# Optimization experiments

Hardware: AMD Instinct MI355X
Metric: run time of the kernel (lower is better)

## Reference

```python
import jax, jax.numpy as jnp
import numpy as np

VOCAB = 50257
MASK_ID = 50256
CLIP = 20.0
GAMMA = 1.0
P_UNIFORM = float(max(np.exp(-CLIP), 0.0))
LOG_B = float(np.clip(-np.log1p((1.0 - P_UNIFORM) / P_UNIFORM * VOCAB / 2.0), -CLIP, None))
B_EXP = float(np.exp(LOG_B))
EPS = 1e-4
B_SZ, SEQ = 4, 512


def setup_inputs() -> dict:
    key = jax.random.key(0)
    k1, k2, k3 = jax.random.split(key, 3)
    input_ids = jax.random.randint(k1, (B_SZ, SEQ), 0, VOCAB)
    t = jax.random.uniform(k2, (B_SZ,), dtype=jnp.float32)
    noise = jax.random.uniform(k3, (B_SZ, SEQ, VOCAB), dtype=jnp.float32)
    return {"input_ids": input_ids, "t": t, "noise": noise}


def _coeffs(t):
    # t: [B] -> per-example blend coefficients, each [B, 1]
    t = t[:, None]
    tg = t ** GAMMA
    t1g = (1.0 - t) ** GAMMA
    c = jnp.sqrt(tg) * jnp.sqrt(t1g) * B_EXP
    C = jnp.clip(tg + t1g + (VOCAB - 2) * c, EPS, None)
    return (t1g - c) / C, c / C, tg / C  # alpha_t, c_t/C_t, t_gamma/C_t


def reference(t, noise, input_ids):
    # Fused form of probs_at_t(one_hot(input_ids), t): since prs is one-hot,
    # probs[b,s,v] = alpha*1{v==id} + c/C, then mask column overwritten to tg/C.
    alpha, cC, mC = _coeffs(t)  # [B,1] each
    col = jnp.arange(VOCAB)[None, None, :]            # [1,1,V]
    hit = col == input_ids[..., None]                 # [B,S,V]
    probs = jnp.where(col == MASK_ID, mC[..., None],
                      jnp.where(hit, (alpha + cC)[..., None], cC[..., None]))
    # Gumbel-max categorical sampling (standard sample_categorical)
    gumbel_norm = 1e-10 - jnp.log(noise + 1e-10)      # [B,S,V]
    z_t = jnp.argmax(probs / gumbel_norm, axis=-1)    # [B,S] int
    return z_t
```

## Files before the change

### kernel.cpp

```cpp
#include <hip/hip_runtime.h>
#include <stdint.h>
#include <stddef.h>


static constexpr int VOCAB   = 50257;
static constexpr int MASK_ID = 50256;
static constexpr double B_EXP_D = 2.061153622438558e-09;

__global__ __launch_bounds__(256) void hd_argmax_kernel(
    const int*   __restrict__ ids,
    const float* __restrict__ tv,
    const float* __restrict__ noise,
    int*         __restrict__ out)
{
    const int row = blockIdx.x;
    const int tid = threadIdx.x;
    const int b   = row >> 9;

    const float t   = tv[b];
    const float tg  = t;
    const float t1g = 1.0f - t;
    const float c   = sqrtf(tg) * sqrtf(t1g) * (float)B_EXP_D;
    float Cd = tg + t1g + 50255.0f * c;
    Cd = fmaxf(Cd, 1e-4f);
    const float pc = c / Cd;
    const float ph = (t1g - c) / Cd + c / Cd;
    const float pm = tg / Cd;
    const int   x  = ids[row];

    const float* __restrict__ rowp = noise + (size_t)row * (size_t)VOCAB;

    const int k     = (4 - (row & 3)) & 3;
    const int nvec  = (VOCAB - k) >> 2;
    const int tail0 = k + (nvec << 2);

    float best = -1.0f;
    int   bidx = 0;

    auto consider = [&](float u, int idx) {
        const float g = 1e-10f - logf(u + 1e-10f);
        const float p = (idx == MASK_ID) ? pm : ((idx == x) ? ph : pc);
        const float r = p / g;
        if (r > best) { best = r; bidx = idx; }
    };

    if (tid < k) consider(rowp[tid], tid);

    const float4* __restrict__ vp = reinterpret_cast<const float4*>(rowp + k);
    for (int i = tid; i < nvec; i += 256) {
        const float4 v = vp[i];
        const int base = k + (i << 2);
        consider(v.x, base);
        consider(v.y, base + 1);
        consider(v.z, base + 2);
        consider(v.w, base + 3);
    }

    if (tid < VOCAB - tail0) consider(rowp[tail0 + tid], tail0 + tid);

    #pragma unroll
    for (int off = 32; off > 0; off >>= 1) {
        const float ov = __shfl_down(best, off, 64);
        const int   oi = __shfl_down(bidx, off, 64);
        if (ov > best || (ov == best && oi < bidx)) { best = ov; bidx = oi; }
    }

    __shared__ float sv[4];
    __shared__ int   si[4];
    const int wid = tid >> 6;
    if ((tid & 63) == 0) { sv[wid] = best; si[wid] = bidx; }
    __syncthreads();
    if (tid == 0) {
        #pragma unroll
        for (int w = 1; w < 4; ++w) {
            if (sv[w] > best || (sv[w] == best && si[w] < bidx)) { best = sv[w]; bidx = si[w]; }
        }
        out[row] = bidx;
    }
}

extern "C" void kernel_launch(void* const* d_in, const int* in_sizes, int n_in,
                              void* d_out, int out_size, void* d_ws, size_t ws_size,
                              hipStream_t stream) {
    const int*   ids   = (const int*)  d_in[0];
    const float* t     = (const float*)d_in[1];
    const float* noise = (const float*)d_in[2];
    int* out = (int*)d_out;

    hd_argmax_kernel<<<dim3(2048), dim3(256), 0, stream>>>(ids, t, noise, out);
}
```

Baseline: 553.9 us.

## Replace per-element log/divide with raw noise argmax over uniform-prob columns

Because every column except the hit id and the mask column has the same probability, and p/g is monotonic in u, the scan now takes a plain argmax of the raw noise while skipping the hit id and the mask column. The log and divide are then applied only to three candidates (best uniform, hit, mask) on thread 0. This removes the transcendental and division work per element, leaving the loop bound by memory bandwidth. Tie-breaking can differ from the reference when float rounding makes distinct u values map to equal ratios.

```diff
diff --git a/kernel.cpp b/kernel.cpp
--- a/kernel.cpp
+++ b/kernel.cpp
@@ -5,6 +5,7 @@
 
 static constexpr int VOCAB   = 50257;
 static constexpr int MASK_ID = 50256;
+static constexpr int NSCAN   = VOCAB - 1;
 static constexpr double B_EXP_D = 2.061153622438558e-09;
 
 __global__ __launch_bounds__(256) void hd_argmax_kernel(
@@ -15,33 +16,19 @@
 {
     const int row = blockIdx.x;
     const int tid = threadIdx.x;
-    const int b   = row >> 9;
-
-    const float t   = tv[b];
-    const float tg  = t;
-    const float t1g = 1.0f - t;
-    const float c   = sqrtf(tg) * sqrtf(t1g) * (float)B_EXP_D;
-    float Cd = tg + t1g + 50255.0f * c;
-    Cd = fmaxf(Cd, 1e-4f);
-    const float pc = c / Cd;
-    const float ph = (t1g - c) / Cd + c / Cd;
-    const float pm = tg / Cd;
-    const int   x  = ids[row];
+    const int x   = ids[row];
 
     const float* __restrict__ rowp = noise + (size_t)row * (size_t)VOCAB;
 
-    const int k     = (4 - (row & 3)) & 3;
-    const int nvec  = (VOCAB - k) >> 2;
+    const int k    = (4 - (row & 3)) & 3;
+    const int nvec = (NSCAN - k) >> 2;
     const int tail0 = k + (nvec << 2);
 
-    float best = -1.0f;
+    float bu   = -1.0f;
     int   bidx = 0;
 
     auto consider = [&](float u, int idx) {
-        const float g = 1e-10f - logf(u + 1e-10f);
-        const float p = (idx == MASK_ID) ? pm : ((idx == x) ? ph : pc);
-        const float r = p / g;
-        if (r > best) { best = r; bidx = idx; }
+        if (u > bu && idx != x) { bu = u; bidx = idx; }
     };
 
     if (tid < k) consider(rowp[tid], tid);
@@ -56,26 +43,51 @@
         consider(v.w, base + 3);
     }
 
-    if (tid < VOCAB - tail0) consider(rowp[tail0 + tid], tail0 + tid);
+    if (tid < NSCAN - tail0) consider(rowp[tail0 + tid], tail0 + tid);
 
     #pragma unroll
     for (int off = 32; off > 0; off >>= 1) {
-        const float ov = __shfl_down(best, off, 64);
+        const float ov = __shfl_down(bu, off, 64);
         const int   oi = __shfl_down(bidx, off, 64);
-        if (ov > best || (ov == best && oi < bidx)) { best = ov; bidx = oi; }
+        if (ov > bu || (ov == bu && oi < bidx)) { bu = ov; bidx = oi; }
     }
 
     __shared__ float sv[4];
     __shared__ int   si[4];
     const int wid = tid >> 6;
-    if ((tid & 63) == 0) { sv[wid] = best; si[wid] = bidx; }
+    if ((tid & 63) == 0) { sv[wid] = bu; si[wid] = bidx; }
     __syncthreads();
+
     if (tid == 0) {
         #pragma unroll
         for (int w = 1; w < 4; ++w) {
-            if (sv[w] > best || (sv[w] == best && si[w] < bidx)) { best = sv[w]; bidx = si[w]; }
+            if (sv[w] > bu || (sv[w] == bu && si[w] < bidx)) { bu = sv[w]; bidx = si[w]; }
         }
-        out[row] = bidx;
+
+        const float t   = tv[row >> 9];
+        const float tg  = t;
+        const float t1g = 1.0f - t;
+        const float c   = sqrtf(tg) * sqrtf(t1g) * (float)B_EXP_D;
+        float Cd = tg + t1g + 50255.0f * c;
+        Cd = fmaxf(Cd, 1e-4f);
+        const float pc = c / Cd;
+        const float ph = (t1g - c) / Cd + c / Cd;
+        const float pm = tg / Cd;
+
+        float best_r = pc / (1e-10f - logf(bu + 1e-10f));
+        int   best_i = bidx;
+
+        if (x != MASK_ID) {
+            const float uh = rowp[x];
+            const float rh = ph / (1e-10f - logf(uh + 1e-10f));
+            if (rh > best_r || (rh == best_r && x < best_i)) { best_r = rh; best_i = x; }
+        }
+        {
+            const float um = rowp[MASK_ID];
+            const float rm = pm / (1e-10f - logf(um + 1e-10f));
+            if (rm > best_r) { best_i = MASK_ID; }
+        }
+        out[row] = best_i;
     }
 }
 
```

New measurement: 536.2 us. -3.2%, faster.
